# Kernel optimization log

Measured on AMD Instinct MI355X. Metric: run time of the kernel, lower is better.

Reference implementation:

```python
import jax, jax.numpy as jnp
import numpy as np

NUM_CAPS = 10       # J: output capsules
PREV_NODES = 16384  # P: input capsules (16*32*32)
IN_CH = 8           # D: input capsule dim
OUT_CH = 16         # O: output capsule dim
BATCH = 32
ROUTING_ITERS = 3


def squash(s):
    # s: (..., O). v = (|s|^2 / (1+|s|^2)) * s / |s|
    sq = jnp.sum(s * s, axis=-1, keepdims=True)
    return s * (sq / ((1.0 + sq) * jnp.sqrt(sq)))


def setup_inputs() -> dict:
    key = jax.random.key(0)
    kx, kw = jax.random.split(key)
    x = jax.random.normal(kx, (BATCH, PREV_NODES, IN_CH), dtype=jnp.float32)
    W = jax.random.normal(kw, (NUM_CAPS, PREV_NODES, IN_CH, OUT_CH), dtype=jnp.float32)
    return {"x": x, "W": W}


def reference(x, W):
    # u_hat[b,j,p,:] = x[b,p,:] @ W[j,p,:,:]  -> (B, J, P, O)
    u_hat = jnp.einsum('bpd,jpdo->bjpo', x, W)
    temp_u_hat = jax.lax.stop_gradient(u_hat)
    B = x.shape[0]
    b = jnp.zeros((B, NUM_CAPS, PREV_NODES, 1), dtype=u_hat.dtype)
    for _ in range(ROUTING_ITERS - 1):
        c = jax.nn.softmax(b, axis=1)                   # over output capsules
        s = jnp.sum(c * temp_u_hat, axis=2)             # (B, J, O)
        v = squash(s)
        uv = jnp.einsum('bjpo,bjo->bjp', temp_u_hat, v)[..., None]
        b = b + uv
    c = jax.nn.softmax(b, axis=1)
    s = jnp.sum(c * u_hat, axis=2)
    v = squash(s)                                       # (B, J, O)
    return v
```

## Files before the change

kernel.cpp:

```cpp
#include <hip/hip_runtime.h>

typedef _Float16 half_t;
typedef half_t h2 __attribute__((ext_vector_type(2)));
typedef half_t h4 __attribute__((ext_vector_type(4)));
typedef float f4 __attribute__((ext_vector_type(4)));

#define J 10
#define P 16384
#define D 8
#define O 16
#define B 32

#define SJO (B * J * O)
#define VL_STRIDE 84

#define PBLK 32
#define NBLK (P / PBLK)

#define WS_VSUM 0
#define WS_VH 20480u
#define WS_WH 32768u
#define WS_XT (WS_WH + 41943040u)
#define WS_PART (WS_XT + 8388608u)
#define WS_NEED (WS_PART + 10485760u)

template <int CTRL>
__device__ __forceinline__ float dpp_mov_f(float v) {
    return __int_as_float(__builtin_amdgcn_update_dpp(
        0, __float_as_int(v), CTRL, 0xF, 0xF, true));
}
__device__ __forceinline__ float row_sum16(float v) {
    v += dpp_mov_f<0xB1>(v);
    v += dpp_mov_f<0x4E>(v);
    v += dpp_mov_f<0x124>(v);
    v += dpp_mov_f<0x128>(v);
    return v;
}

__device__ __forceinline__ h2 pkrtz(float a, float b) {
    return __builtin_bit_cast(h2, __builtin_amdgcn_cvt_pkrtz(a, b));
}

__device__ __forceinline__ float xadd16(float v) {
#if __has_builtin(__builtin_amdgcn_permlane16_swap)
    auto r = __builtin_amdgcn_permlane16_swap(__float_as_uint(v),
                                              __float_as_uint(v), false, false);
    return __uint_as_float(r[0]) + __uint_as_float(r[1]);
#else
    return v + __shfl_xor(v, 16, 64);
#endif
}
__device__ __forceinline__ float xadd32(float v) {
#if __has_builtin(__builtin_amdgcn_permlane32_swap)
    auto r = __builtin_amdgcn_permlane32_swap(__float_as_uint(v),
                                              __float_as_uint(v), false, false);
    return __uint_as_float(r[0]) + __uint_as_float(r[1]);
#else
    return v + __shfl_xor(v, 32, 64);
#endif
}

union U4H { uint4 u; h2 h[4]; };
union U2H { uint2 u2; h2 h[2]; h4 v; };
union U1H { unsigned u; h2 h; };

__global__ __launch_bounds__(256) void wconv(
    const float* __restrict__ W, half_t* __restrict__ Wh)
{
    __shared__ float ls[J][8][132];
    const int t = threadIdx.x;
    const int p0 = blockIdx.x * 8;

#pragma unroll
    for (int it = 0; it < 10; ++it) {
        const int idx = it * 256 + t;
        const int f4i = idx & 31, pp = (idx >> 5) & 7, j = idx >> 8;
        float4 f = *(const float4*)(W + ((size_t)j * P + p0 + pp) * 128 + f4i * 4);
        *(float4*)&ls[j][pp][f4i * 4] = f;
    }
    __syncthreads();
#pragma unroll
    for (int it = 0; it < 5; ++it) {
        const int idx = it * 256 + t;
        const int o = idx & 15, pp = (idx >> 4) & 7, j = idx >> 7;
        U4H pk;
#pragma unroll
        for (int dq = 0; dq < 4; ++dq)
            pk.h[dq] = pkrtz(ls[j][pp][(2 * dq) * 16 + o],
                             ls[j][pp][(2 * dq + 1) * 16 + o]);
        *(uint4*)(Wh + (((size_t)(p0 + pp) * J + j) * 16 + o) * 8) = pk.u;
    }
}

__global__ __launch_bounds__(256) void xconv(
    const float* __restrict__ x, half_t* __restrict__ xt)
{
    __shared__ uint4 xls[64][33];
    const int t = threadIdx.x;
    const int p0 = blockIdx.x * 64;

#pragma unroll
    for (int it = 0; it < 8; ++it) {
        const int idx = it * 256 + t;
        const int pp = idx & 63, b = idx >> 6;
        const float4* xp = (const float4*)(x + ((size_t)b * P + p0 + pp) * 8);
        float4 a = xp[0], c = xp[1];
        U4H pk;
        pk.h[0] = pkrtz(a.x, a.y);
        pk.h[1] = pkrtz(a.z, a.w);
        pk.h[2] = pkrtz(c.x, c.y);
        pk.h[3] = pkrtz(c.z, c.w);
        xls[pp][b] = pk.u;
    }
    __syncthreads();
#pragma unroll
    for (int it = 0; it < 8; ++it) {
        const int idx = it * 256 + t;
        const int b = idx & 31, pp = idx >> 5;
        *(uint4*)(xt + ((size_t)(p0 + pp) * 32 + b) * 8) = xls[pp][b];
    }
}

__global__ __launch_bounds__(512, 4) void caps_pass(
    const half_t* __restrict__ Wh, const half_t* __restrict__ xt,
    const unsigned* __restrict__ vh, float* __restrict__ partial, int first)
{
    __shared__ float s_blk[4 * 16 * 164];
    __shared__ unsigned vls[B * VL_STRIDE];

    const int tid = threadIdx.x;
    const int p0 = blockIdx.x * PBLK;

    if (!first && tid < B * J) {
        const int b = tid / J, j = tid - b * J;
        const uint4* s = (const uint4*)(vh + (size_t)tid * 8);
        uint4* dvl = (uint4*)(vls + b * VL_STRIDE + j * 8);
        dvl[0] = s[0];
        dvl[1] = s[1];
    }

    const int lane = tid & 63;
    const int wv   = tid >> 6;
    const int bh   = wv >> 2;
    const int plg  = wv & 3;
    const int bl16 = lane & 15;
    const int q    = lane >> 4;
    const unsigned kmask = (q < 2) ? 0xFFFFFFFFu : 0u;
    const int vbase = (bh * 16 + bl16) * VL_STRIDE + q * 2;

    __syncthreads();

    f4 acc[J];
#pragma unroll
    for (int j = 0; j < J; ++j) acc[j] = (f4){0.f, 0.f, 0.f, 0.f};
    const f4 zf = (f4){0.f, 0.f, 0.f, 0.f};

    const int pbase = p0 + plg * 8;
#pragma unroll 1
    for (int i = 0; i < 8; ++i) {
        const int p = pbase + i;
        const half_t* wp = Wh + ((size_t)p * J) * 128 + bl16 * 8 + (q & 1) * 4;

        U2H xv;
        xv.u2 = *(const uint2*)(xt + ((size_t)p * 32 + bh * 16 + bl16) * 8
                                + (q & 1) * 4);
        xv.u2.x &= kmask;
        xv.u2.y &= kmask;
        const h4 bfrag = xv.v;

        if (first) {
#pragma unroll
            for (int j = 0; j < J; ++j) {
                const h4 af = *(const h4*)(wp + j * 128);
                f4 u = __builtin_amdgcn_mfma_f32_16x16x16f16(af, bfrag, zf, 0, 0, 0);
#pragma unroll
                for (int r = 0; r < 4; ++r)
                    acc[j][r] = fmaf(0.1f, u[r], acc[j][r]);
            }
        } else {
            h2 uh[J][2];
            float lg[J];
#pragma unroll
            for (int j = 0; j < J; ++j) {
                const h4 af = *(const h4*)(wp + j * 128);
                f4 u = __builtin_amdgcn_mfma_f32_16x16x16f16(af, bfrag, zf, 0, 0, 0);
                uh[j][0] = pkrtz(u[0], u[1]);
                uh[j][1] = pkrtz(u[2], u[3]);
                U2H vf;
                vf.u2 = *(const uint2*)(vls + vbase + j * 8);
                lg[j] = __builtin_amdgcn_fdot2(uh[j][1], vf.h[1],
                        __builtin_amdgcn_fdot2(uh[j][0], vf.h[0], 0.f, false),
                        false);
            }
#pragma unroll
            for (int j = 0; j < J; ++j) lg[j] = xadd16(lg[j]);
#pragma unroll
            for (int j = 0; j < J; ++j) lg[j] = xadd32(lg[j]);
            float Z = 0.f;
#pragma unroll
            for (int j = 0; j < J; ++j) { lg[j] = __expf(lg[j]); Z += lg[j]; }
            const float rZ = __builtin_amdgcn_rcpf(Z);
#pragma unroll
            for (int j = 0; j < J; ++j) {
                const float c = lg[j] * rZ;
                acc[j][0] = fmaf(c, (float)uh[j][0][0], acc[j][0]);
                acc[j][1] = fmaf(c, (float)uh[j][0][1], acc[j][1]);
                acc[j][2] = fmaf(c, (float)uh[j][1][0], acc[j][2]);
                acc[j][3] = fmaf(c, (float)uh[j][1][1], acc[j][3]);
            }
        }
    }

    __syncthreads();
#pragma unroll 1
    for (int r = 0; r < 2; ++r) {
        if (bh == r) {
#pragma unroll
            for (int j = 0; j < J; ++j)
                *(f4*)&s_blk[(size_t)(plg * 16 + bl16) * 164 + j * 16 + 4 * q]
                    = acc[j];
        }
        __syncthreads();
        for (int t = tid; t < 16 * 160; t += 512) {
            const int bl = t / 160, rr = t - bl * 160;
            const float v = s_blk[bl * 164 + rr] + s_blk[(16 + bl) * 164 + rr]
                          + s_blk[(32 + bl) * 164 + rr] + s_blk[(48 + bl) * 164 + rr];
            partial[((size_t)blockIdx.x * 32 + r * 16 + bl) * 160 + rr] = v;
        }
        __syncthreads();
    }
}

__global__ __launch_bounds__(1024) void caps_squash(
    const float* __restrict__ partial, float* __restrict__ Vsum,
    unsigned* __restrict__ vh, float* __restrict__ out, int write_out)
{
    __shared__ float red[4][160];
    const int b = blockIdx.x;
    const int t = threadIdx.x;
    const int o = t & 15, j = (t >> 4) & 15, hf = t >> 8;
    const bool act = j < J;
    const int jo = j * 16 + o;

    if (act) {
        float s = 0.f;
        const float* pp = partial + (size_t)hf * 128 * (32 * 160) + b * 160 + jo;
#pragma unroll 8
        for (int k = 0; k < 128; ++k) s += pp[(size_t)k * (32 * 160)];
        red[hf][jo] = s;
    }
    __syncthreads();
    if (hf == 0) {
        const float s = act ? red[0][jo] + red[1][jo] + red[2][jo] + red[3][jo]
                            : 0.f;
        const float sq = row_sum16(s * s);
        float vnew = 0.f;
        const int idx = (b * J + (act ? j : 0)) * O + o;
        if (act) {
            const float scale = sqrtf(sq) / (1.f + sq);
            const float v = s * scale;
            vnew = Vsum[idx] + v;
            Vsum[idx] = vnew;
            if (write_out) out[idx] = v;
        }
        const float vpart = __shfl_xor(vnew, 1, 64);
        if (act && !(o & 1)) {
            U1H tt; tt.h = pkrtz(vnew, vpart);
            vh[(size_t)(b * J + j) * 8 + (o >> 1)] = tt.u;
        }
    }
}

__global__ __launch_bounds__(256) void caps_zero(float* __restrict__ ws, int n)
{
    const int i = blockIdx.x * 256 + threadIdx.x;
    if (i < n) ws[i] = 0.f;
}

#define FB_PTILE 16
#define FB_NB (P / FB_PTILE)
#define FB_WT_PLS 2576
#define FB_WT_PLH (FB_WT_PLS / 2)
#define FB_XS_OFF (FB_PTILE * FB_WT_PLS)
#define FB_VL_OFF (FB_XS_OFF + FB_PTILE * B * 16)
#define FB_SMEM (FB_VL_OFF + B * VL_STRIDE * 4)

__global__ __launch_bounds__(512, 4) void caps_pass_fb(
    const float* __restrict__ x, const float* __restrict__ W,
    const unsigned* __restrict__ vh, float* __restrict__ s_acc, int first)
{
    __shared__ char smem[FB_SMEM];
    half_t* Wt = (half_t*)smem;
    half_t* xs = (half_t*)(smem + FB_XS_OFF);
    unsigned* vls = (unsigned*)(smem + FB_VL_OFF);
    float* s_blk = (float*)smem;

    const int tid = threadIdx.x;
    const int p0 = blockIdx.x * FB_PTILE;

    {
        const int o4 = tid & 3, d = (tid >> 2) & 7, pl = tid >> 5;
        const float* src = W + (size_t)p0 * (D * O) + (size_t)tid * 4;
        half_t* dst = Wt + pl * FB_WT_PLH + (o4 * 4) * 8 + d;
#pragma unroll
        for (int j = 0; j < J; ++j) {
            float4 f = *(const float4*)(src + (size_t)j * P * (D * O));
            half_t* dj = dst + j * 128;
            dj[0]  = (half_t)f.x;
            dj[8]  = (half_t)f.y;
            dj[16] = (half_t)f.z;
            dj[24] = (half_t)f.w;
        }
    }
    {
        const int bl = tid >> 4, pl = tid & 15;
        const float4* xp = (const float4*)(x + ((size_t)bl * P + p0 + pl) * D);
        float4 a = xp[0], c = xp[1];
        U4H pk;
        pk.h[0] = pkrtz(a.x, a.y);
        pk.h[1] = pkrtz(a.z, a.w);
        pk.h[2] = pkrtz(c.x, c.y);
        pk.h[3] = pkrtz(c.z, c.w);
        *(uint4*)(xs + (size_t)(pl * 16 + bl) * 8) = pk.u;
    }
    if (!first && tid < B * J) {
        const int b = tid / J, j = tid - b * J;
        const uint4* s = (const uint4*)(vh + (size_t)tid * 8);
        uint4* dvl = (uint4*)(vls + b * VL_STRIDE + j * 8);
        dvl[0] = s[0];
        dvl[1] = s[1];
    }

    const int lane = tid & 63;
    const int wv   = tid >> 6;
    const int bh   = wv >> 2;
    const int wid2 = wv & 3;
    const int bl16 = lane & 15;
    const int q    = lane >> 4;
    const unsigned kmask = (q < 2) ? 0xFFFFFFFFu : 0u;
    const int vbase = (bh * 16 + bl16) * VL_STRIDE + q * 2;

    __syncthreads();

    f4 acc[J];
#pragma unroll
    for (int j = 0; j < J; ++j) acc[j] = (f4){0.f, 0.f, 0.f, 0.f};
    const f4 zf = (f4){0.f, 0.f, 0.f, 0.f};

#pragma unroll 1
    for (int pi = 0; pi < 4; ++pi) {
        const int pl = wid2 * 4 + pi;
        U2H xv;
        xv.u2 = *(const uint2*)(xs + (size_t)(pl * 16 + bl16) * 8 + 4 * (q & 1));
        xv.u2.x &= kmask;
        xv.u2.y &= kmask;
        const h4 bfrag = xv.v;
        const half_t* wbase = Wt + pl * FB_WT_PLH + bl16 * 8 + 4 * (q & 1);

        h2 uh[J][2];
        float lg[J];
#pragma unroll
        for (int j = 0; j < J; ++j) {
            const h4 af = *(const h4*)(wbase + j * 128);
            f4 u = __builtin_amdgcn_mfma_f32_16x16x16f16(af, bfrag, zf, 0, 0, 0);
            if (first) {
#pragma unroll
                for (int r = 0; r < 4; ++r)
                    acc[j][r] = fmaf(0.1f, u[r], acc[j][r]);
            } else {
                uh[j][0] = pkrtz(u[0], u[1]);
                uh[j][1] = pkrtz(u[2], u[3]);
                U2H vf;
                vf.u2 = *(const uint2*)(vls + vbase + j * 8);
                lg[j] = __builtin_amdgcn_fdot2(uh[j][1], vf.h[1],
                        __builtin_amdgcn_fdot2(uh[j][0], vf.h[0], 0.f, false),
                        false);
            }
        }
        if (!first) {
#pragma unroll
            for (int j = 0; j < J; ++j) lg[j] = xadd16(lg[j]);
#pragma unroll
            for (int j = 0; j < J; ++j) lg[j] = xadd32(lg[j]);
            float e[J], Z = 0.f;
#pragma unroll
            for (int j = 0; j < J; ++j) { e[j] = __expf(lg[j]); Z += e[j]; }
            const float rZ = __builtin_amdgcn_rcpf(Z);
#pragma unroll
            for (int j = 0; j < J; ++j) {
                const float c = e[j] * rZ;
                acc[j][0] = fmaf(c, (float)uh[j][0][0], acc[j][0]);
                acc[j][1] = fmaf(c, (float)uh[j][0][1], acc[j][1]);
                acc[j][2] = fmaf(c, (float)uh[j][1][0], acc[j][2]);
                acc[j][3] = fmaf(c, (float)uh[j][1][1], acc[j][3]);
            }
        }
    }

    __syncthreads();
#pragma unroll 1
    for (int r = 0; r < 2; ++r) {
        if (bh == r) {
#pragma unroll
            for (int j = 0; j < J; ++j)
                *(f4*)&s_blk[(size_t)(wid2 * 16 + bl16) * 164 + j * 16 + 4 * q]
                    = acc[j];
        }
        __syncthreads();
        for (int t = tid; t < 16 * 160; t += 512) {
            const int bl = t / 160, rr = t - bl * 160;
            const float v = s_blk[bl * 164 + rr] + s_blk[(16 + bl) * 164 + rr]
                          + s_blk[(32 + bl) * 164 + rr] + s_blk[(48 + bl) * 164 + rr];
            atomicAdd(&s_acc[(size_t)(r * 16 + bl) * 160 + rr], v);
        }
        __syncthreads();
    }
}

__global__ __launch_bounds__(256) void caps_squash_fb(
    float* __restrict__ s_acc, float* __restrict__ Vsum,
    unsigned* __restrict__ vh, float* __restrict__ out, int write_out)
{
    const int b = blockIdx.x;
    const int o = threadIdx.x & 15;
    const int j = threadIdx.x >> 4;
    const bool act = j < J;
    const int idx = (b * J + (act ? j : 0)) * O + o;
    float s = act ? s_acc[idx] : 0.f;
    const float sq = row_sum16(s * s);
    float vnew = 0.f;
    if (act) {
        const float scale = sqrtf(sq) / (1.f + sq);
        const float v = s * scale;
        vnew = Vsum[idx] + v;
        Vsum[idx] = vnew;
        s_acc[idx] = 0.f;
        if (write_out) out[idx] = v;
    }
    const float vpart = __shfl_xor(vnew, 1, 64);
    if (act && !(o & 1)) {
        U1H t; t.h = pkrtz(vnew, vpart);
        vh[(size_t)(b * J + j) * 8 + (o >> 1)] = t.u;
    }
}

extern "C" void kernel_launch(void* const* d_in, const int* in_sizes, int n_in,
                              void* d_out, int out_size, void* d_ws, size_t ws_size,
                              hipStream_t stream)
{
    const float* x = (const float*)d_in[0];
    const float* W = (const float*)d_in[1];
    float* out = (float*)d_out;
    char* ws = (char*)d_ws;

    if (ws_size >= WS_NEED) {
        float* Vsum = (float*)(ws + WS_VSUM);
        unsigned* vh = (unsigned*)(ws + WS_VH);
        half_t* Wh = (half_t*)(ws + WS_WH);
        half_t* xt = (half_t*)(ws + WS_XT);
        float* partial = (float*)(ws + WS_PART);

        caps_zero<<<dim3(20), 256, 0, stream>>>(Vsum, SJO);
        wconv<<<dim3(P / 8), 256, 0, stream>>>(W, Wh);
        xconv<<<dim3(P / 64), 256, 0, stream>>>(x, xt);

        for (int it = 0; it < 3; ++it) {
            caps_pass<<<dim3(NBLK), 512, 0, stream>>>(Wh, xt, vh, partial,
                                                      it == 0 ? 1 : 0);
            caps_squash<<<dim3(B), 1024, 0, stream>>>(partial, Vsum, vh, out,
                                                      it == 2 ? 1 : 0);
        }
    } else {
        float* s_acc = (float*)d_ws;
        float* Vsum  = s_acc + SJO;
        unsigned* vh = (unsigned*)(Vsum + SJO);

        caps_zero<<<dim3(40), 256, 0, stream>>>(s_acc, 2 * SJO);
        for (int it = 0; it < 3; ++it) {
            caps_pass_fb<<<dim3(FB_NB), 512, 0, stream>>>(x, W, vh, s_acc,
                                                          it == 0 ? 1 : 0);
            caps_squash_fb<<<dim3(B), 256, 0, stream>>>(s_acc, Vsum, vh, out,
                                                        it == 2 ? 1 : 0);
        }
    }
}
```

Baseline: 238.9 us.

## Stage W and x tiles into LDS via async global_load_lds, halve P block

Each caps_pass block now covers 16 input capsules instead of 32 and prefetches its whole fp16 W and x tiles into shared memory with global_load_lds at kernel start, reusing the s_blk area. The MFMA fragments are then read from LDS rather than straight from global memory. This doubles the number of blocks and partial-sum slices, so the squash reduction reads twice as many partials. The aim is more parallelism and better-overlapped loads, paid for with extra reduction traffic and a larger workspace.

```diff
diff --git a/kernel.cpp b/kernel.cpp
--- a/kernel.cpp
+++ b/kernel.cpp
@@ -14,15 +14,19 @@
 #define SJO (B * J * O)
 #define VL_STRIDE 84
 
-#define PBLK 32
+#define PBLK 16
 #define NBLK (P / PBLK)
+
+#define XT_OFF 40960
+#define VL_OFF 49152
+#define SMEM_BYTES (VL_OFF + B * VL_STRIDE * 4)
 
 #define WS_VSUM 0
 #define WS_VH 20480u
 #define WS_WH 32768u
 #define WS_XT (WS_WH + 41943040u)
 #define WS_PART (WS_XT + 8388608u)
-#define WS_NEED (WS_PART + 10485760u)
+#define WS_NEED (WS_PART + 20971520u)
 
 template <int CTRL>
 __device__ __forceinline__ float dpp_mov_f(float v) {
@@ -58,6 +62,12 @@
 #else
     return v + __shfl_xor(v, 32, 64);
 #endif
+}
+
+__device__ __forceinline__ void gl_lds16(const void* g, void* l) {
+    __builtin_amdgcn_global_load_lds(
+        (const __attribute__((address_space(1))) unsigned int*)g,
+        (__attribute__((address_space(3))) unsigned int*)l, 16, 0, 0);
 }
 
 union U4H { uint4 u; h2 h[4]; };
@@ -125,12 +135,25 @@
     const half_t* __restrict__ Wh, const half_t* __restrict__ xt,
     const unsigned* __restrict__ vh, float* __restrict__ partial, int first)
 {
-    __shared__ float s_blk[4 * 16 * 164];
-    __shared__ unsigned vls[B * VL_STRIDE];
+    __shared__ char smem[SMEM_BYTES];
+    unsigned* vls = (unsigned*)(smem + VL_OFF);
+    float* s_blk = (float*)smem;
 
     const int tid = threadIdx.x;
+    const int lane = tid & 63;
+    const int wv   = tid >> 6;
     const int p0 = blockIdx.x * PBLK;
 
+    {
+        const char* wsrc = (const char*)Wh + (size_t)p0 * 2560;
+        const char* xsrc = (const char*)xt + (size_t)p0 * 512;
+        const int chunk = wv * 1024;
+        const int loff  = lane * 16;
+#pragma unroll
+        for (int r = 0; r < 5; ++r)
+            gl_lds16(wsrc + r * 8192 + chunk + loff, smem + r * 8192 + chunk);
+        gl_lds16(xsrc + chunk + loff, smem + XT_OFF + chunk);
+    }
     if (!first && tid < B * J) {
         const int b = tid / J, j = tid - b * J;
         const uint4* s = (const uint4*)(vh + (size_t)tid * 8);
@@ -139,8 +162,6 @@
         dvl[1] = s[1];
     }
 
-    const int lane = tid & 63;
-    const int wv   = tid >> 6;
     const int bh   = wv >> 2;
     const int plg  = wv & 3;
     const int bl16 = lane & 15;
@@ -150,28 +171,31 @@
 
     __syncthreads();
 
+    const half_t* Wl = (const half_t*)smem;
+    const half_t* xl = (const half_t*)(smem + XT_OFF);
+
     f4 acc[J];
 #pragma unroll
     for (int j = 0; j < J; ++j) acc[j] = (f4){0.f, 0.f, 0.f, 0.f};
     const f4 zf = (f4){0.f, 0.f, 0.f, 0.f};
 
-    const int pbase = p0 + plg * 8;
 #pragma unroll 1
-    for (int i = 0; i < 8; ++i) {
-        const int p = pbase + i;
-        const half_t* wp = Wh + ((size_t)p * J) * 128 + bl16 * 8 + (q & 1) * 4;
+    for (int i = 0; i < 4; ++i) {
+        const int pl = plg * 4 + i;
 
         U2H xv;
-        xv.u2 = *(const uint2*)(xt + ((size_t)p * 32 + bh * 16 + bl16) * 8
+        xv.u2 = *(const uint2*)(xl + ((size_t)pl * 32 + bh * 16 + bl16) * 8
                                 + (q & 1) * 4);
         xv.u2.x &= kmask;
         xv.u2.y &= kmask;
         const h4 bfrag = xv.v;
 
+        const half_t* wbase = Wl + (size_t)pl * 1280 + bl16 * 8 + (q & 1) * 4;
+
         if (first) {
 #pragma unroll
             for (int j = 0; j < J; ++j) {
-                const h4 af = *(const h4*)(wp + j * 128);
+                const h4 af = *(const h4*)(wbase + j * 128);
                 f4 u = __builtin_amdgcn_mfma_f32_16x16x16f16(af, bfrag, zf, 0, 0, 0);
 #pragma unroll
                 for (int r = 0; r < 4; ++r)
@@ -182,7 +206,7 @@
             float lg[J];
 #pragma unroll
             for (int j = 0; j < J; ++j) {
-                const h4 af = *(const h4*)(wp + j * 128);
+                const h4 af = *(const h4*)(wbase + j * 128);
                 f4 u = __builtin_amdgcn_mfma_f32_16x16x16f16(af, bfrag, zf, 0, 0, 0);
                 uh[j][0] = pkrtz(u[0], u[1]);
                 uh[j][1] = pkrtz(u[2], u[3]);
@@ -244,9 +268,9 @@
 
     if (act) {
         float s = 0.f;
-        const float* pp = partial + (size_t)hf * 128 * (32 * 160) + b * 160 + jo;
+        const float* pp = partial + (size_t)hf * 256 * (32 * 160) + b * 160 + jo;
 #pragma unroll 8
-        for (int k = 0; k < 128; ++k) s += pp[(size_t)k * (32 * 160)];
+        for (int k = 0; k < 256; ++k) s += pp[(size_t)k * (32 * 160)];
         red[hf][jo] = s;
     }
     __syncthreads();
```

New measurement: 263.5 us. +10.3%, slower.
